# Kernel optimization log

Measured on AMD Instinct MI355X. Metric: run time of the kernel, lower is better.

The kernel has to match this reference:

```python
import jax, jax.numpy as jnp
import numpy as np

B = 256        # batch of LLR frames
N = 576        # code length (from wman_N0576_R34_z24)
MR = 144       # check rows = N * (1 - 3/4)
Z = 24         # lifting factor
IT = 3         # decoding iterations
ROW_DEG = 15   # check-node degree (WiMAX rate-3/4)


def setup_inputs() -> dict:
    key = jax.random.key(0)
    r = jax.random.normal(key, (B, N), dtype=jnp.float32)
    # Deterministic sparse Tanner graph: 15 ones per check row (>=2 required for top-2)
    rng = np.random.RandomState(0)
    Hnp = np.zeros((MR, N), dtype=np.int32)
    cols = np.argsort(rng.rand(MR, N), axis=1)[:, :ROW_DEG]
    Hnp[np.arange(MR)[:, None], cols] = 1
    H = jnp.asarray(Hnp)
    alpha = jnp.ones((MR // Z, N // Z, IT), dtype=jnp.float32) * 0.7
    beta = jnp.ones((MR // Z, N // Z, IT), dtype=jnp.float32) * 0.05
    return {"r": r, "alpha": alpha, "beta": beta, "H": H}


def _decode(r, alpha, beta, Hf):
    # r: (B, N) channel LLRs; Hf: (MR, N) float 0/1 parity-check mask
    mask = Hf == 1.0
    node = jnp.arange(N)[None, None, :]           # (1, 1, N)
    M = Hf[None, :, :] * r[:, None, :]            # initial v->c messages (B, MR, N)
    E = jnp.zeros_like(M)
    n_it = alpha.shape[-1]
    for it in range(n_it):
        a = jnp.repeat(jnp.repeat(alpha[:, :, it], Z, axis=0), Z, axis=1)  # (MR, N)
        bt = jnp.repeat(jnp.repeat(beta[:, :, it], Z, axis=0), Z, axis=1)  # (MR, N)
        # check -> variable: masked min-2 magnitude + extrinsic sign product
        abs_M = jnp.abs(M)
        masked = jnp.where(mask, abs_M, jnp.inf)
        neg_vals, idx = jax.lax.top_k(-masked, 2)  # two smallest per check row
        min_vals = -neg_vals                        # (B, MR, 2)
        # exclude self: use 2nd min at the argmin position, 1st min elsewhere
        E_abs = jnp.where(node == idx[..., 0:1], min_vals[..., 1:2], min_vals[..., 0:1])
        signs = jnp.where(mask, jnp.sign(M), 1.0)
        row_sign_prod = jnp.prod(signs, axis=2, keepdims=True)
        E_sign = row_sign_prod * signs              # extrinsic sign
        E = a * E_sign * jax.nn.relu(E_abs - bt) * Hf
        # variable -> check: sum-minus-self
        sum_E = jnp.sum(E, axis=1, keepdims=True)   # (B, 1, N)
        M = (r[:, None, :] + sum_E - E) * Hf
    return r + jnp.sum(E, axis=1)                   # posterior LLRs (B, N)


def reference(r, alpha, beta, H):
    return _decode(r, alpha, beta, H.astype(jnp.float32))
```

## Files before the change

kernel.cpp:

```cpp
#include <hip/hip_runtime.h>

#define BATCH   256
#define NCOL    576
#define MROW    144
#define ZLIFT   24
#define NIT     3
#define ROW_DEG 15
#define PKSTR   16
#define NSCIT   ((MROW/ZLIFT) * (NCOL/ZLIFT) * NIT)
#define TPB     576
#define CCAP    18
#define CSTR    19

__global__ __launch_bounds__(256) void build_cols_kernel(
    const int* __restrict__ H, int* __restrict__ pk)
{
    const int wave = (blockIdx.x * blockDim.x + threadIdx.x) >> 6;
    const int lane = threadIdx.x & 63;
    if (wave >= MROW) return;
    const int4* row4 = (const int4*)(H + (size_t)wave * NCOL);
    const int srow = (wave / ZLIFT) * (NCOL / ZLIFT);
    const unsigned long long below = (1ull << lane) - 1ull;
    if (lane == 0) pk[wave * PKSTR + 15] = 0;
    int base = 0;
    #pragma unroll
    for (int r0 = 0; r0 < 3; ++r0) {
        const int vidx = r0 * 64 + lane;
        int4 h = make_int4(0, 0, 0, 0);
        if (vidx < NCOL / 4) h = row4[vidx];
        const int b0 = h.x != 0, b1 = h.y != 0, b2 = h.z != 0, b3 = h.w != 0;
        const unsigned long long m0 = __ballot(b0);
        const unsigned long long m1 = __ballot(b1);
        const unsigned long long m2 = __ballot(b2);
        const unsigned long long m3 = __ballot(b3);
        const int cnt_below = __popcll(m0 & below) + __popcll(m1 & below)
                            + __popcll(m2 & below) + __popcll(m3 & below);
        const int bits[4] = {b0, b1, b2, b3};
        const int n0 = vidx * 4;
        int pref = 0;
        #pragma unroll
        for (int c = 0; c < 4; ++c) {
            if (bits[c]) {
                const int idx = base + cnt_below + pref;
                const int n = n0 + c;
                if (idx < ROW_DEG)
                    pk[wave * PKSTR + idx] = n | ((srow + n / ZLIFT) << 16);
                ++pref;
            }
        }
        base += __popcll(m0) + __popcll(m1) + __popcll(m2) + __popcll(m3);
    }
}

__global__ __launch_bounds__(TPB) void ldpc_decode_kernel(
    const float* __restrict__ r,
    const float* __restrict__ alpha,
    const float* __restrict__ beta,
    const int*   __restrict__ pk,
    float*       __restrict__ out)
{
    __shared__ float  r_s[NCOL];
    __shared__ float  colsum[NCOL];
    __shared__ float  E_s[NCOL * CSTR];
    __shared__ float2 ab_s[NSCIT];
    __shared__ int    cdeg[NCOL];

    const int b   = blockIdx.x;
    const int tid = threadIdx.x;
    const int row = tid >> 2;
    const int sub = tid & 3;

    r_s[tid]  = r[(size_t)b * NCOL + tid];
    cdeg[tid] = 0;
    #pragma unroll
    for (int j = 0; j < CSTR; ++j) E_s[j * NCOL + tid] = 0.0f;
    if (tid < NSCIT) ab_s[tid] = make_float2(alpha[tid], beta[tid]);
    __syncthreads();

    const int4 q = *(const int4*)(pk + row * PKSTR + sub * 4);
    int pk_r[4] = {q.x, q.y, q.z, q.w};
    float r_r[4], E_r[4];
    int   slot_r[4];
    #pragma unroll
    for (int j = 0; j < 4; ++j) {
        const int kglob = sub * 4 + j;
        const int n = pk_r[j] & 0xFFFF;
        r_r[j] = r_s[n];
        E_r[j] = 0.0f;
        if (kglob < ROW_DEG)
            slot_r[j] = n * CSTR + atomicAdd(&cdeg[n], 1);
    }

    for (int it = 0; it < NIT; ++it) {
        float vals[4];
        float min1 = INFINITY, min2 = INFINITY;
        int   kmin = 1 << 30;
        float sprod = 1.0f;
        #pragma unroll
        for (int j = 0; j < 4; ++j) {
            const int kglob = sub * 4 + j;
            const bool val = (kglob < ROW_DEG);
            float v;
            if (it == 0) {
                v = r_r[j];
            } else {
                const int n = pk_r[j] & 0xFFFF;
                v = r_r[j] + colsum[n] - E_r[j];
            }
            vals[j] = v;
            const float av = val ? fabsf(v) : INFINITY;
            const float s = val ? ((v > 0.0f) ? 1.0f : ((v < 0.0f) ? -1.0f : 0.0f))
                                : 1.0f;
            sprod *= s;
            if (av < min1)      { min2 = min1; min1 = av; kmin = kglob; }
            else if (av < min2) { min2 = av; }
        }
        #pragma unroll
        for (int m = 1; m <= 2; m <<= 1) {
            const float o1 = __shfl_xor(min1, m);
            const float o2 = __shfl_xor(min2, m);
            const int   ok = __shfl_xor(kmin, m);
            const float os = __shfl_xor(sprod, m);
            const bool self_lo = ((sub & m) == 0);
            const float lo1 = self_lo ? min1 : o1;
            const float lo2 = self_lo ? min2 : o2;
            const int   lok = self_lo ? kmin : ok;
            const float hi1 = self_lo ? o1 : min1;
            const float hi2 = self_lo ? o2 : min2;
            const int   hik = self_lo ? ok : kmin;
            if (hi1 < lo1) { min1 = hi1; kmin = hik; min2 = fminf(hi2, lo1); }
            else           { min1 = lo1; kmin = lok; min2 = fminf(lo2, hi1); }
            sprod *= os;
        }
        #pragma unroll
        for (int j = 0; j < 4; ++j) {
            const int kglob = sub * 4 + j;
            if (kglob < ROW_DEG) {
                const int sidx = pk_r[j] >> 16;
                const float v = vals[j];
                const float s = (v > 0.0f) ? 1.0f : ((v < 0.0f) ? -1.0f : 0.0f);
                const float2 ab = ab_s[sidx * NIT + it];
                const float eabs = (kglob == kmin) ? min2 : min1;
                float mag = eabs - ab.y;
                if (mag < 0.0f) mag = 0.0f;
                const float E = ab.x * (sprod * s) * mag;
                E_r[j] = E;
                E_s[slot_r[j]] = E;
            }
        }
        __syncthreads();

        const float* base = &E_s[tid * CSTR];
        float sum = 0.0f;
        #pragma unroll
        for (int i = 0; i < CCAP; ++i) sum += base[i];
        if (it < NIT - 1) {
            colsum[tid] = sum;
            __syncthreads();
        } else {
            out[(size_t)b * NCOL + tid] = r_s[tid] + sum;
        }
    }
}

extern "C" void kernel_launch(void* const* d_in, const int* in_sizes, int n_in,
                              void* d_out, int out_size, void* d_ws, size_t ws_size,
                              hipStream_t stream) {
    const float* r     = (const float*)d_in[0];
    const float* alpha = (const float*)d_in[1];
    const float* beta  = (const float*)d_in[2];
    const int*   H     = (const int*)d_in[3];
    float* out = (float*)d_out;
    int*   pk  = (int*)d_ws;

    build_cols_kernel<<<(MROW * 64 + 255) / 256, 256, 0, stream>>>(H, pk);
    ldpc_decode_kernel<<<BATCH, TPB, 0, stream>>>(r, alpha, beta, pk, out);
}
```

Baseline: 65.58 us.

## Replace per-column E slot buffer with shared-memory atomicAdd column sums

Replaces the padded per-column E_s slot array (filled per slot, then reduced by each column thread) with float atomicAdd into triple-buffered column-sum arrays in LDS. This drops the large LDS zero-init, the slot-assignment atomics and the 18-element gather reduction, and removes one barrier per iteration. The iteration scale factor is premultiplied into the packed index. The cost is LDS float-atomic contention on shared columns and a summation order that is no longer deterministic.

```diff
diff --git a/kernel.cpp b/kernel.cpp
--- a/kernel.cpp
+++ b/kernel.cpp
@@ -9,8 +9,6 @@
 #define PKSTR   16
 #define NSCIT   ((MROW/ZLIFT) * (NCOL/ZLIFT) * NIT)
 #define TPB     576
-#define CCAP    18
-#define CSTR    19
 
 __global__ __launch_bounds__(256) void build_cols_kernel(
     const int* __restrict__ H, int* __restrict__ pk)
@@ -44,7 +42,7 @@
                 const int idx = base + cnt_below + pref;
                 const int n = n0 + c;
                 if (idx < ROW_DEG)
-                    pk[wave * PKSTR + idx] = n | ((srow + n / ZLIFT) << 16);
+                    pk[wave * PKSTR + idx] = n | (((srow + n / ZLIFT) * NIT) << 16);
                 ++pref;
             }
         }
@@ -60,38 +58,31 @@
     float*       __restrict__ out)
 {
     __shared__ float  r_s[NCOL];
-    __shared__ float  colsum[NCOL];
-    __shared__ float  E_s[NCOL * CSTR];
+    __shared__ float  cs0[NCOL];
+    __shared__ float  cs1[NCOL];
+    __shared__ float  cs2[NCOL];
     __shared__ float2 ab_s[NSCIT];
-    __shared__ int    cdeg[NCOL];
 
     const int b   = blockIdx.x;
     const int tid = threadIdx.x;
     const int row = tid >> 2;
     const int sub = tid & 3;
 
-    r_s[tid]  = r[(size_t)b * NCOL + tid];
-    cdeg[tid] = 0;
-    #pragma unroll
-    for (int j = 0; j < CSTR; ++j) E_s[j * NCOL + tid] = 0.0f;
+    r_s[tid] = r[(size_t)b * NCOL + tid];
+    cs0[tid] = 0.0f;
+    cs1[tid] = 0.0f;
+    cs2[tid] = 0.0f;
     if (tid < NSCIT) ab_s[tid] = make_float2(alpha[tid], beta[tid]);
     __syncthreads();
 
     const int4 q = *(const int4*)(pk + row * PKSTR + sub * 4);
-    int pk_r[4] = {q.x, q.y, q.z, q.w};
-    float r_r[4], E_r[4];
-    int   slot_r[4];
+    int   pk_r[4] = {q.x, q.y, q.z, q.w};
+    float r_r[4], E_r[4] = {0.0f, 0.0f, 0.0f, 0.0f};
     #pragma unroll
-    for (int j = 0; j < 4; ++j) {
-        const int kglob = sub * 4 + j;
-        const int n = pk_r[j] & 0xFFFF;
-        r_r[j] = r_s[n];
-        E_r[j] = 0.0f;
-        if (kglob < ROW_DEG)
-            slot_r[j] = n * CSTR + atomicAdd(&cdeg[n], 1);
-    }
+    for (int j = 0; j < 4; ++j)
+        r_r[j] = r_s[pk_r[j] & 0xFFFF];
 
-    for (int it = 0; it < NIT; ++it) {
+    auto check = [&](const float* prev, float* next, const int it) {
         float vals[4];
         float min1 = INFINITY, min2 = INFINITY;
         int   kmin = 1 << 30;
@@ -100,13 +91,8 @@
         for (int j = 0; j < 4; ++j) {
             const int kglob = sub * 4 + j;
             const bool val = (kglob < ROW_DEG);
-            float v;
-            if (it == 0) {
-                v = r_r[j];
-            } else {
-                const int n = pk_r[j] & 0xFFFF;
-                v = r_r[j] + colsum[n] - E_r[j];
-            }
+            float v = r_r[j];
+            if (prev) v += prev[pk_r[j] & 0xFFFF] - E_r[j];
             vals[j] = v;
             const float av = val ? fabsf(v) : INFINITY;
             const float s = val ? ((v > 0.0f) ? 1.0f : ((v < 0.0f) ? -1.0f : 0.0f))
@@ -136,31 +122,27 @@
         for (int j = 0; j < 4; ++j) {
             const int kglob = sub * 4 + j;
             if (kglob < ROW_DEG) {
-                const int sidx = pk_r[j] >> 16;
                 const float v = vals[j];
                 const float s = (v > 0.0f) ? 1.0f : ((v < 0.0f) ? -1.0f : 0.0f);
-                const float2 ab = ab_s[sidx * NIT + it];
+                const float2 ab = ab_s[(pk_r[j] >> 16) + it];
                 const float eabs = (kglob == kmin) ? min2 : min1;
                 float mag = eabs - ab.y;
                 if (mag < 0.0f) mag = 0.0f;
                 const float E = ab.x * (sprod * s) * mag;
                 E_r[j] = E;
-                E_s[slot_r[j]] = E;
+                atomicAdd(&next[pk_r[j] & 0xFFFF], E);
             }
         }
-        __syncthreads();
+    };
 
-        const float* base = &E_s[tid * CSTR];
-        float sum = 0.0f;
-        #pragma unroll
-        for (int i = 0; i < CCAP; ++i) sum += base[i];
-        if (it < NIT - 1) {
-            colsum[tid] = sum;
-            __syncthreads();
-        } else {
-            out[(size_t)b * NCOL + tid] = r_s[tid] + sum;
-        }
-    }
+    check(nullptr, cs1, 0);
+    __syncthreads();
+    check(cs1, cs0, 1);
+    __syncthreads();
+    check(cs0, cs2, 2);
+    __syncthreads();
+
+    out[(size_t)b * NCOL + tid] = r_s[tid] + cs2[tid];
 }
 
 extern "C" void kernel_launch(void* const* d_in, const int* in_sizes, int n_in,
```

Result: slower. 72.62 us (+10.7%).
